# Kernel optimization log

Measured on AMD Instinct MI355X. Metric: run time of the kernel, lower is better.

The kernel has to match this reference:

```python
import jax, jax.numpy as jnp
import numpy as np

B, H, W, C = 8, 64, 64, 256  # N = H*W = 4096, pooled length N//2 = 2048


def setup_inputs() -> dict:
    key = jax.random.key(0)
    k1, k2, k3, k4 = jax.random.split(key, 4)
    scale = np.sqrt(2.0 / C).astype(np.float32)  # he_normal for 1x1 conv
    return {
        "x": jax.random.normal(k1, (B, H, W, C), dtype=jnp.float32),
        "w_theta": jax.random.normal(k2, (C, C), dtype=jnp.float32) * scale,
        "w_phi": jax.random.normal(k3, (C, C), dtype=jnp.float32) * scale,
        "w_g": jax.random.normal(k4, (C, C), dtype=jnp.float32) * scale,
    }


def _maxpool1d(z):
    # MaxPool1D(pool_size=2, strides=2, padding='valid') over axis 1
    b, n, c = z.shape
    return jnp.max(z.reshape(b, n // 2, 2, c), axis=2)


def reference(x, w_theta, w_phi, w_g):
    b, h, w, c = x.shape
    n = h * w
    xf = x.reshape(b, n, c)                       # [B, N, C]
    theta = xf @ w_theta                          # [B, N, C] (1x1 conv)
    phi = _maxpool1d(xf @ w_phi)                  # [B, N//2, C]
    f = jnp.einsum('bnc,bmc->bnm', theta, phi)    # [B, N, N//2] affinity
    f = jax.nn.softmax(f, axis=-1)
    g = _maxpool1d(xf @ w_g)                      # [B, N//2, C]
    y = jnp.einsum('bnm,bmc->bnc', f, g)          # [B, N, C]
    y = y.reshape(b, h, w, c)
    return x + y                                  # residual
```

## Files before the change

### kernel.cpp

```cpp
#include <hip/hip_runtime.h>
#include <stdint.h>

#define CC 256
#define NN 4096
#define MM 2048
#define BB 8
#define NROWS (BB*NN)
#define PROWS (BB*MM)

typedef __attribute__((ext_vector_type(8))) short    short8;
typedef __attribute__((ext_vector_type(8))) _Float16 half8;
typedef __attribute__((ext_vector_type(4))) float    float4v;

__device__ __forceinline__ unsigned short f2bf(float f) {
    unsigned int u = __float_as_uint(f);
    u += 0x7fffu + ((u >> 16) & 1u);
    return (unsigned short)(u >> 16);
}
__device__ __forceinline__ float bf2f(unsigned short h) {
    return __uint_as_float(((unsigned int)h) << 16);
}
__device__ __forceinline__ unsigned short f2h(float f) {
    union { _Float16 h; unsigned short u; } cv; cv.h = (_Float16)f; return cv.u;
}
__device__ __forceinline__ float h2f(unsigned short u) {
    union { _Float16 h; unsigned short u; } cv; cv.u = u; return (float)cv.h;
}

__global__ __launch_bounds__(256) void xsplit_kernel(
    const float* __restrict__ x,
    unsigned short* __restrict__ x_hi,
    unsigned short* __restrict__ x_lo)
{
    const size_t i = ((size_t)blockIdx.x*256 + threadIdx.x) * 8;
    float4v a0 = *(const float4v*)(x + i);
    float4v a1 = *(const float4v*)(x + i + 4);
    short8 h, l;
    #pragma unroll
    for (int j = 0; j < 4; ++j) {
        unsigned short h0 = f2bf(a0[j]);
        h[j]   = (short)h0; l[j]   = (short)f2bf(a0[j] - bf2f(h0));
        unsigned short h1 = f2bf(a1[j]);
        h[4+j] = (short)h1; l[4+j] = (short)f2bf(a1[j] - bf2f(h1));
    }
    *(short8*)(x_hi + i) = h;
    *(short8*)(x_lo + i) = l;
}

__global__ void wsplit_kernel(const float* __restrict__ w_theta,
                              const float* __restrict__ w_phi,
                              const float* __restrict__ w_g,
                              unsigned short* __restrict__ wT_hi,
                              unsigned short* __restrict__ wT_lo)
{
    __shared__ float tile[64][65];
    const int widx = blockIdx.z;
    const int kt = blockIdx.x, ct = blockIdx.y;
    const float* w = (widx == 0) ? w_theta : (widx == 1) ? w_phi : w_g;
    const int t  = threadIdx.x;
    const int tc = t & 63, tr = t >> 6;
    #pragma unroll
    for (int i = 0; i < 16; ++i) {
        const int lk = tr*16 + i;
        tile[lk][tc] = w[(size_t)(kt*64 + lk)*CC + ct*64 + tc];
    }
    __syncthreads();
    #pragma unroll
    for (int i = 0; i < 16; ++i) {
        const int lc = tr*16 + i;
        float v = tile[tc][lc];
        const int c = ct*64 + lc, k = kt*64 + tc;
        unsigned short hh = f2bf(v);
        size_t o = ((size_t)widx*CC + c)*CC + k;
        wT_hi[o] = hh;
        wT_lo[o] = f2bf(v - bf2f(hh));
    }
}

__global__ __launch_bounds__(256, 4) void proj_kernel(
    const unsigned short* __restrict__ x_hi,
    const unsigned short* __restrict__ x_lo,
    const unsigned short* __restrict__ wT_hi,
    const unsigned short* __restrict__ wT_lo,
    unsigned short* __restrict__ th,
    unsigned short* __restrict__ ph,
    unsigned short* __restrict__ g_t)
{
    __shared__ unsigned short wt_hi[64*136];
    __shared__ unsigned short wt_lo[64*136];

    const int tid  = threadIdx.x;
    const int rb   = blockIdx.x & 511;
    const int cv   = blockIdx.x >> 9;
    const int r0   = rb * 64;
    const int widx = cv >> 2;
    const int wc0  = (cv & 3) * 64;
    const unsigned short* wThp = wT_hi + ((size_t)widx*CC + wc0)*CC;
    const unsigned short* wTlp = wT_lo + ((size_t)widx*CC + wc0)*CC;
    const bool split3 = (widx < 2);

    const int wv   = tid >> 6;
    const int lane = tid & 63;
    const int quad = lane >> 4;
    const int l15  = lane & 15;
    const int arow = r0 + wv*16 + l15;
    const unsigned short* axh = x_hi + (size_t)arow*CC + quad*8;
    const unsigned short* axl = x_lo + (size_t)arow*CC + quad*8;

    float4v acc[4];
    #pragma unroll
    for (int nf = 0; nf < 4; ++nf) acc[nf] = (float4v){0.f,0.f,0.f,0.f};

    for (int h = 0; h < 2; ++h) {
        __syncthreads();
        {
            const int j    = tid & 63;
            const int kseg = tid >> 6;
            const size_t base = (size_t)j*CC + h*128 + kseg*32;
            const unsigned short* sh = wThp + base;
            unsigned short* dh = &wt_hi[j*136 + kseg*32];
            #pragma unroll
            for (int u = 0; u < 4; ++u)
                *(uint4*)(dh + u*8) = *(const uint4*)(sh + u*8);
            if (split3) {
                const unsigned short* sl = wTlp + base;
                unsigned short* dl = &wt_lo[j*136 + kseg*32];
                #pragma unroll
                for (int u = 0; u < 4; ++u)
                    *(uint4*)(dl + u*8) = *(const uint4*)(sl + u*8);
            }
        }
        __syncthreads();

        #pragma unroll
        for (int ks = 0; ks < 4; ++ks) {
            short8 a_hi = *(const short8*)(axh + h*128 + ks*32);
            short8 a_lo;
            if (split3) a_lo = *(const short8*)(axl + h*128 + ks*32);
            #pragma unroll
            for (int nf = 0; nf < 4; ++nf) {
                const int wrow = nf*16 + l15;
                short8 b_hi = *(const short8*)&wt_hi[wrow*136 + ks*32 + quad*8];
                acc[nf] = __builtin_amdgcn_mfma_f32_16x16x32_bf16(a_hi, b_hi, acc[nf], 0,0,0);
                if (split3) {
                    short8 b_lo = *(const short8*)&wt_lo[wrow*136 + ks*32 + quad*8];
                    acc[nf] = __builtin_amdgcn_mfma_f32_16x16x32_bf16(a_hi, b_lo, acc[nf], 0,0,0);
                    acc[nf] = __builtin_amdgcn_mfma_f32_16x16x32_bf16(a_lo, b_hi, acc[nf], 0,0,0);
                }
            }
        }
    }

    const int rowbase = r0 + wv*16 + quad*4;
    if (widx == 0) {
        #pragma unroll
        for (int nf = 0; nf < 4; ++nf) {
            const int c = wc0 + nf*16 + l15;
            #pragma unroll
            for (int r = 0; r < 4; ++r)
                th[(size_t)(rowbase + r)*CC + c] = f2h(acc[nf][r]);
        }
    } else if (widx == 1) {
        #pragma unroll
        for (int nf = 0; nf < 4; ++nf) {
            const int c = wc0 + nf*16 + l15;
            #pragma unroll
            for (int rp = 0; rp < 2; ++rp) {
                float v = fmaxf(acc[nf][2*rp], acc[nf][2*rp+1]);
                const int prow = rowbase/2 + rp;
                ph[(size_t)prow*CC + c] = f2h(v);
            }
        }
    } else {
        #pragma unroll
        for (int nf = 0; nf < 4; ++nf) {
            const int c = wc0 + nf*16 + l15;
            #pragma unroll
            for (int rp = 0; rp < 2; ++rp) {
                float v = fmaxf(acc[nf][2*rp], acc[nf][2*rp+1]);
                const int prow = rowbase/2 + rp;
                const int b = prow >> 11;
                const int m = prow & 2047;
                g_t[((size_t)b*CC + c)*MM + m] = f2bf(v);
            }
        }
    }
}

__global__ void phimean_kernel(const unsigned short* __restrict__ ph,
                               float* __restrict__ phbar)
{
    const int b = blockIdx.x >> 6, chunk = blockIdx.x & 63;
    const int c = threadIdx.x;
    const size_t base = ((size_t)b*MM + chunk*32)*CC + c;
    float s = 0.f;
    for (int r = 0; r < 32; ++r) s += h2f(ph[base + (size_t)r*CC]);
    atomicAdd(&phbar[b*CC + c], s * (1.0f/MM));
}

__global__ __launch_bounds__(256, 3) void attn_kernel(
    const float* __restrict__ x,
    const unsigned short* __restrict__ th,
    const unsigned short* __restrict__ ph,
    const unsigned short* __restrict__ g_t,
    const float* __restrict__ phbar,
    float* __restrict__ out)
{
    __shared__ unsigned short s_ph[2][32*264];
    __shared__ unsigned short s_p[4][16*40];
    __shared__ float          s_l[64];

    const int tid  = threadIdx.x;
    const int q0   = blockIdx.x * 64;
    const int b    = q0 >> 12;
    const int wv   = tid >> 6;
    const int lane = tid & 63;
    const int quad = lane >> 4;
    const int l15  = lane & 15;

    const int sti = tid >> 3;
    const int stc = (tid & 7) * 32;
    const size_t phbase = (size_t)b * MM * CC;
    const unsigned short* stsrc = ph + phbase + (size_t)sti*CC + stc;

    half8 t_hi[8];
    {
        const unsigned short* bh = th + (size_t)(q0 + wv*16 + l15)*CC;
        #pragma unroll
        for (int ks = 0; ks < 8; ++ks)
            t_hi[ks] = *(const half8*)(bh + ks*32 + quad*8);
    }

    float sh128[4];
    {
        float sp = 0.f;
        #pragma unroll
        for (int ks = 0; ks < 8; ++ks) {
            const int k0 = ks*32 + quad*8;
            float4v m0 = *(const float4v*)&phbar[b*CC + k0];
            float4v m1 = *(const float4v*)&phbar[b*CC + k0 + 4];
            #pragma unroll
            for (int j = 0; j < 4; ++j) {
                sp += (float)t_hi[ks][j]   * m0[j];
                sp += (float)t_hi[ks][4+j] * m1[j];
            }
        }
        sp += __shfl_xor(sp, 16);
        sp += __shfl_xor(sp, 32);
        #pragma unroll
        for (int r = 0; r < 4; ++r)
            sh128[r] = __shfl(sp, quad*4 + r) + 128.f;
    }

    float4v O[4][4];
    #pragma unroll
    for (int rt = 0; rt < 4; ++rt)
        #pragma unroll
        for (int ct = 0; ct < 4; ++ct) O[rt][ct] = (float4v){0.f,0.f,0.f,0.f};
    float4v accl = (float4v){0.f,0.f,0.f,0.f};

    short8 ones;
    #pragma unroll
    for (int j = 0; j < 8; ++j) ones[j] = (short)0x3F80;

    const unsigned short* gl =
        g_t + ((size_t)b*CC + wv*64 + l15)*MM + quad*8;

    {
        unsigned short* dh = &s_ph[0][sti*264 + stc];
        #pragma unroll
        for (int u = 0; u < 4; ++u)
            *(uint4*)(dh + u*8) = *(const uint4*)(stsrc + u*8);
    }
    __syncthreads();

    for (int kt = 0; kt < 64; ++kt) {
        const int key0 = kt * 32;
        const int cur  = kt & 1;

        uint4 stg[4];
        if (kt < 63) {
            const unsigned short* sn = stsrc + (size_t)(key0 + 32)*CC;
            #pragma unroll
            for (int u = 0; u < 4; ++u) stg[u] = *(const uint4*)(sn + u*8);
        }
        short8 gf[4];
        #pragma unroll
        for (int ct = 0; ct < 4; ++ct)
            gf[ct] = *(const short8*)(gl + (size_t)ct*16*MM + key0);

        float4v S0 = (float4v){0.f,0.f,0.f,0.f};
        float4v S1 = (float4v){0.f,0.f,0.f,0.f};
        #pragma unroll
        for (int ks = 0; ks < 8; ++ks) {
            half8 b0 = *(const half8*)&s_ph[cur][( 0 + l15)*264 + ks*32 + quad*8];
            half8 b1 = *(const half8*)&s_ph[cur][(16 + l15)*264 + ks*32 + quad*8];
            S0 = __builtin_amdgcn_mfma_f32_16x16x32_f16(t_hi[ks], b0, S0, 0,0,0);
            S1 = __builtin_amdgcn_mfma_f32_16x16x32_f16(t_hi[ks], b1, S1, 0,0,0);
        }

        unsigned short* pw = &s_p[wv][0];
        #pragma unroll
        for (int r = 0; r < 4; ++r) {
            float a0 = fminf(fmaxf(S0[r] - sh128[r], -85.f), 85.f);
            float a1 = fminf(fmaxf(S1[r] - sh128[r], -85.f), 85.f);
            pw[(quad*4 + r)*40 + l15]      = f2bf(__expf(a0));
            pw[(quad*4 + r)*40 + 16 + l15] = f2bf(__expf(a1));
        }
        asm volatile("s_waitcnt lgkmcnt(0)" ::: "memory");
        short8 pown = *(const short8*)&s_p[wv][l15*40 + quad*8];
        accl = __builtin_amdgcn_mfma_f32_16x16x32_bf16(pown, ones, accl, 0,0,0);

        if (kt < 63) {
            unsigned short* dh = &s_ph[cur ^ 1][sti*264 + stc];
            #pragma unroll
            for (int u = 0; u < 4; ++u) *(uint4*)(dh + u*8) = stg[u];
        }
        __syncthreads();

        #pragma unroll
        for (int rt = 0; rt < 4; ++rt) {
            short8 pA = *(const short8*)&s_p[rt][l15*40 + quad*8];
            #pragma unroll
            for (int ct = 0; ct < 4; ++ct)
                O[rt][ct] = __builtin_amdgcn_mfma_f32_16x16x32_bf16(pA, gf[ct], O[rt][ct], 0,0,0);
        }
        __syncthreads();
    }

    if (l15 == 0) {
        #pragma unroll
        for (int r = 0; r < 4; ++r) s_l[wv*16 + quad*4 + r] = accl[r];
    }
    __syncthreads();

    #pragma unroll
    for (int rt = 0; rt < 4; ++rt) {
        #pragma unroll
        for (int r = 0; r < 4; ++r) {
            const int row = q0 + rt*16 + quad*4 + r;
            const float rl = 1.0f / s_l[rt*16 + quad*4 + r];
            #pragma unroll
            for (int ct = 0; ct < 4; ++ct) {
                const int c = wv*64 + ct*16 + l15;
                const size_t idx = (size_t)row*CC + c;
                out[idx] = x[idx] + O[rt][ct][r] * rl;
            }
        }
    }
}

extern "C" void kernel_launch(void* const* d_in, const int* in_sizes, int n_in,
                              void* d_out, int out_size, void* d_ws, size_t ws_size,
                              hipStream_t stream) {
    const float* x       = (const float*)d_in[0];
    const float* w_theta = (const float*)d_in[1];
    const float* w_phi   = (const float*)d_in[2];
    const float* w_g     = (const float*)d_in[3];
    float* out = (float*)d_out;

    unsigned short* th    = (unsigned short*)d_ws;
    unsigned short* ph    = th    + (size_t)NROWS*CC;
    unsigned short* g_t   = ph    + (size_t)PROWS*CC;
    unsigned short* x_hi  = g_t   + (size_t)PROWS*CC;
    unsigned short* x_lo  = x_hi  + (size_t)NROWS*CC;
    unsigned short* wT_hi = x_lo  + (size_t)NROWS*CC;
    unsigned short* wT_lo = wT_hi + (size_t)3*CC*CC;
    float*          phbar = (float*)(wT_lo + (size_t)3*CC*CC);

    hipMemsetAsync(phbar, 0, BB*CC*sizeof(float), stream);
    xsplit_kernel<<<NROWS*CC/8/256, 256, 0, stream>>>(x, x_hi, x_lo);
    wsplit_kernel<<<dim3(4,4,3), 256, 0, stream>>>(w_theta, w_phi, w_g, wT_hi, wT_lo);
    proj_kernel<<<6144, 256, 0, stream>>>(x_hi, x_lo, wT_hi, wT_lo, th, ph, g_t);
    phimean_kernel<<<512, 256, 0, stream>>>(ph, phbar);
    attn_kernel<<<NROWS/64, 256, 0, stream>>>(x, th, ph, g_t, phbar, out);
}
```

Before: 285.6 us.

## Software-pipeline attention loop: compute next tile's scores while accumulating current PV

Restructures the attention key-tile loop into a software pipeline. A prologue computes the first tile's probabilities. Each iteration then runs the next tile's QK^T and exp alongside the current tile's P·G MFMAs, using a double-buffered probability buffer. Global prefetch of phi moves two tiles ahead and G fragments are loaded one tile ahead. This drops one __syncthreads per iteration. The extra live registers (next-tile G fragments, scores) force launch bounds down from 3 to 2 waves per SIMD, trading occupancy for instruction-level overlap.

After: 372.4 us. 30.4% more time.

```diff
diff --git a/kernel.cpp b/kernel.cpp
--- a/kernel.cpp
+++ b/kernel.cpp
@@ -198,7 +198,7 @@
     atomicAdd(&phbar[b*CC + c], s * (1.0f/MM));
 }
 
-__global__ __launch_bounds__(256, 3) void attn_kernel(
+__global__ __launch_bounds__(256, 2) void attn_kernel(
     const float* __restrict__ x,
     const unsigned short* __restrict__ th,
     const unsigned short* __restrict__ ph,
@@ -207,7 +207,7 @@
     float* __restrict__ out)
 {
     __shared__ unsigned short s_ph[2][32*264];
-    __shared__ unsigned short s_p[4][16*40];
+    __shared__ unsigned short s_p2[2][4][16*40];
     __shared__ float          s_l[64];
 
     const int tid  = threadIdx.x;
@@ -274,32 +274,27 @@
     }
     __syncthreads();
 
-    for (int kt = 0; kt < 64; ++kt) {
-        const int key0 = kt * 32;
-        const int cur  = kt & 1;
-
+    short8 gfc[4];
+    #pragma unroll
+    for (int ct = 0; ct < 4; ++ct)
+        gfc[ct] = *(const short8*)(gl + (size_t)ct*16*MM);
+    {
         uint4 stg[4];
-        if (kt < 63) {
-            const unsigned short* sn = stsrc + (size_t)(key0 + 32)*CC;
+        {
+            const unsigned short* sn = stsrc + (size_t)32*CC;
             #pragma unroll
             for (int u = 0; u < 4; ++u) stg[u] = *(const uint4*)(sn + u*8);
         }
-        short8 gf[4];
-        #pragma unroll
-        for (int ct = 0; ct < 4; ++ct)
-            gf[ct] = *(const short8*)(gl + (size_t)ct*16*MM + key0);
-
         float4v S0 = (float4v){0.f,0.f,0.f,0.f};
         float4v S1 = (float4v){0.f,0.f,0.f,0.f};
         #pragma unroll
         for (int ks = 0; ks < 8; ++ks) {
-            half8 b0 = *(const half8*)&s_ph[cur][( 0 + l15)*264 + ks*32 + quad*8];
-            half8 b1 = *(const half8*)&s_ph[cur][(16 + l15)*264 + ks*32 + quad*8];
+            half8 b0 = *(const half8*)&s_ph[0][( 0 + l15)*264 + ks*32 + quad*8];
+            half8 b1 = *(const half8*)&s_ph[0][(16 + l15)*264 + ks*32 + quad*8];
             S0 = __builtin_amdgcn_mfma_f32_16x16x32_f16(t_hi[ks], b0, S0, 0,0,0);
             S1 = __builtin_amdgcn_mfma_f32_16x16x32_f16(t_hi[ks], b1, S1, 0,0,0);
         }
-
-        unsigned short* pw = &s_p[wv][0];
+        unsigned short* pw = &s_p2[0][wv][0];
         #pragma unroll
         for (int r = 0; r < 4; ++r) {
             float a0 = fminf(fmaxf(S0[r] - sh128[r], -85.f), 85.f);
@@ -308,23 +303,77 @@
             pw[(quad*4 + r)*40 + 16 + l15] = f2bf(__expf(a1));
         }
         asm volatile("s_waitcnt lgkmcnt(0)" ::: "memory");
-        short8 pown = *(const short8*)&s_p[wv][l15*40 + quad*8];
+        short8 pown = *(const short8*)&s_p2[0][wv][l15*40 + quad*8];
         accl = __builtin_amdgcn_mfma_f32_16x16x32_bf16(pown, ones, accl, 0,0,0);
-
+        unsigned short* dh = &s_ph[1][sti*264 + stc];
+        #pragma unroll
+        for (int u = 0; u < 4; ++u) *(uint4*)(dh + u*8) = stg[u];
+    }
+    __syncthreads();
+
+    for (int kt = 0; kt < 64; ++kt) {
+        const int cur  = kt & 1;
+        const int nx   = cur ^ 1;
+        const int key0 = kt * 32;
+
+        uint4 stg[4];
+        if (kt < 62) {
+            const unsigned short* sn = stsrc + (size_t)(key0 + 64)*CC;
+            #pragma unroll
+            for (int u = 0; u < 4; ++u) stg[u] = *(const uint4*)(sn + u*8);
+        }
+        short8 gfn[4];
         if (kt < 63) {
-            unsigned short* dh = &s_ph[cur ^ 1][sti*264 + stc];
+            #pragma unroll
+            for (int ct = 0; ct < 4; ++ct)
+                gfn[ct] = *(const short8*)(gl + (size_t)ct*16*MM + key0 + 32);
+        }
+
+        float4v S0 = (float4v){0.f,0.f,0.f,0.f};
+        float4v S1 = (float4v){0.f,0.f,0.f,0.f};
+        if (kt < 63) {
+            #pragma unroll
+            for (int ks = 0; ks < 8; ++ks) {
+                half8 b0 = *(const half8*)&s_ph[nx][( 0 + l15)*264 + ks*32 + quad*8];
+                half8 b1 = *(const half8*)&s_ph[nx][(16 + l15)*264 + ks*32 + quad*8];
+                S0 = __builtin_amdgcn_mfma_f32_16x16x32_f16(t_hi[ks], b0, S0, 0,0,0);
+                S1 = __builtin_amdgcn_mfma_f32_16x16x32_f16(t_hi[ks], b1, S1, 0,0,0);
+            }
+        }
+
+        #pragma unroll
+        for (int rt = 0; rt < 4; ++rt) {
+            short8 pA = *(const short8*)&s_p2[cur][rt][l15*40 + quad*8];
+            #pragma unroll
+            for (int ct = 0; ct < 4; ++ct)
+                O[rt][ct] = __builtin_amdgcn_mfma_f32_16x16x32_bf16(pA, gfc[ct], O[rt][ct], 0,0,0);
+        }
+
+        if (kt < 63) {
+            unsigned short* pw = &s_p2[nx][wv][0];
+            #pragma unroll
+            for (int r = 0; r < 4; ++r) {
+                float a0 = fminf(fmaxf(S0[r] - sh128[r], -85.f), 85.f);
+                float a1 = fminf(fmaxf(S1[r] - sh128[r], -85.f), 85.f);
+                pw[(quad*4 + r)*40 + l15]      = f2bf(__expf(a0));
+                pw[(quad*4 + r)*40 + 16 + l15] = f2bf(__expf(a1));
+            }
+            asm volatile("s_waitcnt lgkmcnt(0)" ::: "memory");
+            short8 pown = *(const short8*)&s_p2[nx][wv][l15*40 + quad*8];
+            accl = __builtin_amdgcn_mfma_f32_16x16x32_bf16(pown, ones, accl, 0,0,0);
+        }
+
+        if (kt < 62) {
+            unsigned short* dh = &s_ph[cur][sti*264 + stc];
             #pragma unroll
             for (int u = 0; u < 4; ++u) *(uint4*)(dh + u*8) = stg[u];
         }
-        __syncthreads();
-
-        #pragma unroll
-        for (int rt = 0; rt < 4; ++rt) {
-            short8 pA = *(const short8*)&s_p[rt][l15*40 + quad*8];
-            #pragma unroll
-            for (int ct = 0; ct < 4; ++ct)
-                O[rt][ct] = __builtin_amdgcn_mfma_f32_16x16x32_bf16(pA, gf[ct], O[rt][ct], 0,0,0);
-        }
+
+        if (kt < 63) {
+            #pragma unroll
+            for (int ct = 0; ct < 4; ++ct) gfc[ct] = gfn[ct];
+        }
+
         __syncthreads();
     }
 
```

## Split attention over key halves and merge partial sums in a combine kernel

Applied to the files above, without the earlier changes.

The attention kernel now splits the 2048 keys into two halves, so each block handles one half and twice as many blocks run. Each block writes its unnormalised partial output and row sums to workspace, reusing the x_hi and wT_hi regions, with the second half going straight into out. A new combine kernel adds the two partials, normalises, and adds the residual. This works because the softmax uses a fixed shift rather than a running max. The launch bound also moves from 3 to 4 blocks per CU. The cost is extra global traffic for the partial outputs, one more launch, and the risk that wT_hi is too small to hold the row-sum buffer.

Result: slower. 355.7 us (+24.5%).

```diff
diff --git a/kernel.cpp b/kernel.cpp
--- a/kernel.cpp
+++ b/kernel.cpp
@@ -198,21 +198,26 @@
     atomicAdd(&phbar[b*CC + c], s * (1.0f/MM));
 }
 
-__global__ __launch_bounds__(256, 3) void attn_kernel(
-    const float* __restrict__ x,
+__global__ __launch_bounds__(256, 4) void attn_kernel(
     const unsigned short* __restrict__ th,
     const unsigned short* __restrict__ ph,
     const unsigned short* __restrict__ g_t,
     const float* __restrict__ phbar,
-    float* __restrict__ out)
+    float* __restrict__ o0,
+    float* __restrict__ o1,
+    float* __restrict__ lb)
 {
     __shared__ unsigned short s_ph[2][32*264];
     __shared__ unsigned short s_p[4][16*40];
-    __shared__ float          s_l[64];
 
     const int tid  = threadIdx.x;
-    const int q0   = blockIdx.x * 64;
-    const int b    = q0 >> 12;
+    const int bb   = blockIdx.x & 7;
+    const int rest = blockIdx.x >> 3;
+    const int qt   = rest >> 1;
+    const int kh   = rest & 1;
+    const int q0   = bb*NN + qt*64;
+    const int b    = bb;
+    const int kbase = kh * 1024;
     const int wv   = tid >> 6;
     const int lane = tid & 63;
     const int quad = lane >> 4;
@@ -221,7 +226,7 @@
     const int sti = tid >> 3;
     const int stc = (tid & 7) * 32;
     const size_t phbase = (size_t)b * MM * CC;
-    const unsigned short* stsrc = ph + phbase + (size_t)sti*CC + stc;
+    const unsigned short* stsrc = ph + phbase + (size_t)(kbase + sti)*CC + stc;
 
     half8 t_hi[8];
     {
@@ -274,13 +279,13 @@
     }
     __syncthreads();
 
-    for (int kt = 0; kt < 64; ++kt) {
-        const int key0 = kt * 32;
+    for (int kt = 0; kt < 32; ++kt) {
+        const int key0 = kbase + kt * 32;
         const int cur  = kt & 1;
 
         uint4 stg[4];
-        if (kt < 63) {
-            const unsigned short* sn = stsrc + (size_t)(key0 + 32)*CC;
+        if (kt < 31) {
+            const unsigned short* sn = stsrc + (size_t)(kt*32 + 32)*CC;
             #pragma unroll
             for (int u = 0; u < 4; ++u) stg[u] = *(const uint4*)(sn + u*8);
         }
@@ -311,7 +316,7 @@
         short8 pown = *(const short8*)&s_p[wv][l15*40 + quad*8];
         accl = __builtin_amdgcn_mfma_f32_16x16x32_bf16(pown, ones, accl, 0,0,0);
 
-        if (kt < 63) {
+        if (kt < 31) {
             unsigned short* dh = &s_ph[cur ^ 1][sti*264 + stc];
             #pragma unroll
             for (int u = 0; u < 4; ++u) *(uint4*)(dh + u*8) = stg[u];
@@ -328,26 +333,50 @@
         __syncthreads();
     }
 
+    float* od = (kh == 0) ? o0 : o1;
     if (l15 == 0) {
         #pragma unroll
-        for (int r = 0; r < 4; ++r) s_l[wv*16 + quad*4 + r] = accl[r];
-    }
-    __syncthreads();
+        for (int r = 0; r < 4; ++r)
+            lb[(size_t)kh*NROWS + q0 + wv*16 + quad*4 + r] = accl[r];
+    }
 
     #pragma unroll
     for (int rt = 0; rt < 4; ++rt) {
         #pragma unroll
         for (int r = 0; r < 4; ++r) {
             const int row = q0 + rt*16 + quad*4 + r;
-            const float rl = 1.0f / s_l[rt*16 + quad*4 + r];
             #pragma unroll
             for (int ct = 0; ct < 4; ++ct) {
                 const int c = wv*64 + ct*16 + l15;
-                const size_t idx = (size_t)row*CC + c;
-                out[idx] = x[idx] + O[rt][ct][r] * rl;
-            }
-        }
-    }
+                od[(size_t)row*CC + c] = O[rt][ct][r];
+            }
+        }
+    }
+}
+
+__global__ __launch_bounds__(256) void combine_kernel(
+    const float* __restrict__ x,
+    const float* __restrict__ o0,
+    const float* __restrict__ lb,
+    float* __restrict__ out)
+{
+    const size_t i = ((size_t)blockIdx.x*256 + threadIdx.x) * 8;
+    const int row = (int)(i >> 8);
+    const float rl = 1.0f / (lb[row] + lb[NROWS + row]);
+    float4v x0 = *(const float4v*)(x + i);
+    float4v x1 = *(const float4v*)(x + i + 4);
+    float4v a0 = *(const float4v*)(o0 + i);
+    float4v a1 = *(const float4v*)(o0 + i + 4);
+    float4v b0 = *(const float4v*)(out + i);
+    float4v b1 = *(const float4v*)(out + i + 4);
+    float4v r0, r1;
+    #pragma unroll
+    for (int j = 0; j < 4; ++j) {
+        r0[j] = x0[j] + (a0[j] + b0[j]) * rl;
+        r1[j] = x1[j] + (a1[j] + b1[j]) * rl;
+    }
+    *(float4v*)(out + i)     = r0;
+    *(float4v*)(out + i + 4) = r1;
 }
 
 extern "C" void kernel_launch(void* const* d_in, const int* in_sizes, int n_in,
@@ -368,10 +397,14 @@
     unsigned short* wT_lo = wT_hi + (size_t)3*CC*CC;
     float*          phbar = (float*)(wT_lo + (size_t)3*CC*CC);
 
+    float* o0 = (float*)x_hi;
+    float* lb = (float*)wT_hi;
+
     hipMemsetAsync(phbar, 0, BB*CC*sizeof(float), stream);
     xsplit_kernel<<<NROWS*CC/8/256, 256, 0, stream>>>(x, x_hi, x_lo);
     wsplit_kernel<<<dim3(4,4,3), 256, 0, stream>>>(w_theta, w_phi, w_g, wT_hi, wT_lo);
     proj_kernel<<<6144, 256, 0, stream>>>(x_hi, x_lo, wT_hi, wT_lo, th, ph, g_t);
     phimean_kernel<<<512, 256, 0, stream>>>(ph, phbar);
-    attn_kernel<<<NROWS/64, 256, 0, stream>>>(x, th, ph, g_t, phbar, out);
-}
+    attn_kernel<<<NROWS/64*2, 256, 0, stream>>>(th, ph, g_t, phbar, o0, out, lb);
+    combine_kernel<<<NROWS*CC/2048, 256, 0, stream>>>(x, o0, lb, out);
+}
```

## Store g in MFMA fragment order and interleave attention blocks across batches

Applied to the files above, without the earlier changes.

The g projection output is now written in a pre-swizzled fragment layout, so each lane in the attention kernel loads its 8-element MFMA operand from one contiguous 1 KB-per-fragment region instead of doing strided per-row loads from a transposed array. The attention grid mapping also interleaves batches across consecutive blocks, which changes which blocks run concurrently and how they share phi/g in L2. The cost is scattered 2-byte stores in the projection kernel and an L2 sharing pattern that differs from the previous batch-contiguous order.

Result: faster. 270.8 us (-5.2%).

```diff
diff --git a/kernel.cpp b/kernel.cpp
--- a/kernel.cpp
+++ b/kernel.cpp
@@ -84,7 +84,7 @@
     const unsigned short* __restrict__ wT_lo,
     unsigned short* __restrict__ th,
     unsigned short* __restrict__ ph,
-    unsigned short* __restrict__ g_t)
+    unsigned short* __restrict__ g_f)
 {
     __shared__ unsigned short wt_hi[64*136];
     __shared__ unsigned short wt_lo[64*136];
@@ -175,13 +175,19 @@
         #pragma unroll
         for (int nf = 0; nf < 4; ++nf) {
             const int c = wc0 + nf*16 + l15;
+            const int ct = c >> 4;
+            const int c15 = c & 15;
             #pragma unroll
             for (int rp = 0; rp < 2; ++rp) {
                 float v = fmaxf(acc[nf][2*rp], acc[nf][2*rp+1]);
                 const int prow = rowbase/2 + rp;
-                const int b = prow >> 11;
-                const int m = prow & 2047;
-                g_t[((size_t)b*CC + c)*MM + m] = f2bf(v);
+                const int b  = prow >> 11;
+                const int m  = prow & 2047;
+                const int kt = m >> 5;
+                const int km = m & 31;
+                const int lane_t = (km >> 3)*16 + c15;
+                const int j = km & 7;
+                g_f[(((size_t)(b*64 + kt)*16 + ct)*64 + lane_t)*8 + j] = f2bf(v);
             }
         }
     }
@@ -202,7 +208,7 @@
     const float* __restrict__ x,
     const unsigned short* __restrict__ th,
     const unsigned short* __restrict__ ph,
-    const unsigned short* __restrict__ g_t,
+    const unsigned short* __restrict__ g_f,
     const float* __restrict__ phbar,
     float* __restrict__ out)
 {
@@ -211,8 +217,10 @@
     __shared__ float          s_l[64];
 
     const int tid  = threadIdx.x;
-    const int q0   = blockIdx.x * 64;
-    const int b    = q0 >> 12;
+    const int bb   = blockIdx.x & 7;
+    const int qt   = blockIdx.x >> 3;
+    const int q0   = bb*NN + qt*64;
+    const int b    = bb;
     const int wv   = tid >> 6;
     const int lane = tid & 63;
     const int quad = lane >> 4;
@@ -263,8 +271,7 @@
     #pragma unroll
     for (int j = 0; j < 8; ++j) ones[j] = (short)0x3F80;
 
-    const unsigned short* gl =
-        g_t + ((size_t)b*CC + wv*64 + l15)*MM + quad*8;
+    const unsigned short* glf = g_f + (size_t)b*MM*CC + (size_t)lane*8;
 
     {
         unsigned short* dh = &s_ph[0][sti*264 + stc];
@@ -287,7 +294,7 @@
         short8 gf[4];
         #pragma unroll
         for (int ct = 0; ct < 4; ++ct)
-            gf[ct] = *(const short8*)(gl + (size_t)ct*16*MM + key0);
+            gf[ct] = *(const short8*)(glf + (size_t)(kt*16 + wv*4 + ct)*512);
 
         float4v S0 = (float4v){0.f,0.f,0.f,0.f};
         float4v S1 = (float4v){0.f,0.f,0.f,0.f};
@@ -361,8 +368,8 @@
 
     unsigned short* th    = (unsigned short*)d_ws;
     unsigned short* ph    = th    + (size_t)NROWS*CC;
-    unsigned short* g_t   = ph    + (size_t)PROWS*CC;
-    unsigned short* x_hi  = g_t   + (size_t)PROWS*CC;
+    unsigned short* g_f   = ph    + (size_t)PROWS*CC;
+    unsigned short* x_hi  = g_f   + (size_t)PROWS*CC;
     unsigned short* x_lo  = x_hi  + (size_t)NROWS*CC;
     unsigned short* wT_hi = x_lo  + (size_t)NROWS*CC;
     unsigned short* wT_lo = wT_hi + (size_t)3*CC*CC;
@@ -371,7 +378,7 @@
     hipMemsetAsync(phbar, 0, BB*CC*sizeof(float), stream);
     xsplit_kernel<<<NROWS*CC/8/256, 256, 0, stream>>>(x, x_hi, x_lo);
     wsplit_kernel<<<dim3(4,4,3), 256, 0, stream>>>(w_theta, w_phi, w_g, wT_hi, wT_lo);
-    proj_kernel<<<6144, 256, 0, stream>>>(x_hi, x_lo, wT_hi, wT_lo, th, ph, g_t);
+    proj_kernel<<<6144, 256, 0, stream>>>(x_hi, x_lo, wT_hi, wT_lo, th, ph, g_f);
     phimean_kernel<<<512, 256, 0, stream>>>(ph, phbar);
-    attn_kernel<<<NROWS/64, 256, 0, stream>>>(x, th, ph, g_t, phbar, out);
-}
+    attn_kernel<<<NROWS/64, 256, 0, stream>>>(x, th, ph, g_f, phbar, out);
+}
```
